# Kernel tuning notes

Measured on AMD Instinct MI355X. Metric: run time of the kernel, lower is better.

Reference implementation:

```python
import jax, jax.numpy as jnp
import numpy as np

N_NODES = 100000
N_EDGES = 1600000
D_IN, D_HID, D_OUT = 128, 128, 40


def _sgconv(feat, W, b, src, dst, n_nodes):
    # DGL SGConv, k=1, norm='both': D^{-1/2} A D^{-1/2} X W + b
    ones = jnp.ones(dst.shape, dtype=feat.dtype)
    deg = jax.ops.segment_sum(ones, dst, num_segments=n_nodes)  # in-degrees
    norm = jnp.clip(deg, 1.0) ** -0.5  # [N]
    h = feat * norm[:, None]
    # sparse aggregation: gather from src, scatter-add to dst
    h = jax.ops.segment_sum(h[src], dst, num_segments=n_nodes)  # [N, d]
    h = h * norm[:, None]
    return h @ W + b


def setup_inputs() -> dict:
    key = jax.random.key(0)
    ks = jax.random.split(key, 6)
    features = jax.random.normal(ks[0], (N_NODES, D_IN), dtype=jnp.float32)
    src = jax.random.randint(ks[1], (N_EDGES,), 0, N_NODES, dtype=jnp.int32)
    dst = jax.random.randint(ks[2], (N_EDGES,), 0, N_NODES, dtype=jnp.int32)
    # Xavier-uniform init like DGL's fc
    lim1 = float(np.sqrt(6.0 / (D_IN + D_HID)))
    lim2 = float(np.sqrt(6.0 / (D_HID + D_OUT)))
    W1 = jax.random.uniform(ks[3], (D_IN, D_HID), jnp.float32, -lim1, lim1)
    b1 = jnp.zeros((D_HID,), dtype=jnp.float32)
    W2 = jax.random.uniform(ks[4], (D_HID, D_OUT), jnp.float32, -lim2, lim2)
    b2 = jnp.zeros((D_OUT,), dtype=jnp.float32)
    return {"features": features, "src": src, "dst": dst,
            "W1": W1, "b1": b1, "W2": W2, "b2": b2, "n_nodes": N_NODES}


def reference(features, src, dst, W1, b1, W2, b2, n_nodes):
    x = _sgconv(features, W1, b1, src, dst, n_nodes)
    x = jax.nn.elu(x)
    x = _sgconv(x, W2, b2, src, dst, n_nodes)
    return x
```

## Files before the change

kernel.cpp:

```cpp
#include <hip/hip_runtime.h>
#include <hip/hip_fp16.h>
#include <math.h>


#define DIN  128
#define DHID 128
#define DOUT 40
#define BSHIFT 9
#define BNODES 512

union U8  { uint2 u; __half2 h[2]; };
union U16 { uint4 u; __half2 h[4]; };

typedef _Float16 f16x8 __attribute__((ext_vector_type(8)));
typedef float    f32x4 __attribute__((ext_vector_type(4)));
union F16X8 { uint4 u; f16x8 f; };
union HCV   { __half h; unsigned short s; };

__device__ __forceinline__ float elu_f(float x) {
    return x > 0.0f ? x : (expf(x) - 1.0f);
}


__global__ void pass1_bucket(const int* __restrict__ src, const int* __restrict__ dst,
                             int E, int NB, int cap,
                             int* __restrict__ bcur, int* __restrict__ bbuf) {
    __shared__ int cnt[256];
    __shared__ int wcur[256];
    const int CHUNK = 8192;
    for (long base = (long)blockIdx.x * CHUNK; base < E; base += (long)gridDim.x * CHUNK) {
        int n = min(CHUNK, (int)(E - base));
        if (threadIdx.x < 256) cnt[threadIdx.x] = 0;
        __syncthreads();
        for (int i = threadIdx.x; i < n; i += blockDim.x) {
            int b = dst[base + i] >> BSHIFT;
            atomicAdd(&cnt[b], 1);
        }
        __syncthreads();
        if (threadIdx.x < NB) {
            int c = cnt[threadIdx.x];
            wcur[threadIdx.x] = (c > 0) ? atomicAdd(&bcur[threadIdx.x], c) : 0;
        }
        __syncthreads();
        for (int i = threadIdx.x; i < n; i += blockDim.x) {
            int s = src[base + i];
            int d = dst[base + i];
            int b = d >> BSHIFT;
            int slot = atomicAdd(&wcur[b], 1);
            if (slot < cap) bbuf[(long)b * cap + slot] = (s << BSHIFT) | (d & (BNODES - 1));
        }
        __syncthreads();
    }
}

__global__ void bucket_scan(const int* __restrict__ bcur, int* __restrict__ bbase, int NB) {
    if (blockIdx.x == 0 && threadIdx.x == 0) {
        int run = 0;
        for (int b = 0; b < NB; ++b) { bbase[b] = run; run += bcur[b]; }
        bbase[NB] = run;
    }
}

__global__ void pass2_sort(const int* __restrict__ bbuf, const int* __restrict__ bcur,
                           const int* __restrict__ bbase, int N, int NB, int cap,
                           float* __restrict__ norm, int* __restrict__ rowptr,
                           int* __restrict__ esrc) {
    __shared__ int cnt[BNODES];
    int b = blockIdx.x;
    int n_b = min(bcur[b], cap);
    int gbase = bbase[b];
    int dbase = b << BSHIFT;
    const int* eb = bbuf + (long)b * cap;
    for (int i = threadIdx.x; i < BNODES; i += blockDim.x) cnt[i] = 0;
    __syncthreads();
    for (int i = threadIdx.x; i < n_b; i += blockDim.x)
        atomicAdd(&cnt[eb[i] & (BNODES - 1)], 1);
    __syncthreads();
    for (int i = threadIdx.x; i < BNODES; i += blockDim.x) {
        int d = dbase + i;
        if (d < N) norm[d] = rsqrtf(fmaxf((float)cnt[i], 1.0f));
    }
    __syncthreads();
    if (threadIdx.x == 0) {
        int run = 0;
        #pragma unroll 4
        for (int i = 0; i < BNODES; ++i) { int c = cnt[i]; cnt[i] = run; run += c; }
    }
    __syncthreads();
    for (int i = threadIdx.x; i < BNODES; i += blockDim.x) {
        int d = dbase + i;
        if (d < N) rowptr[d] = gbase + cnt[i];
    }
    if (b == NB - 1 && threadIdx.x == 0) rowptr[N] = bbase[NB];
    __syncthreads();
    for (int i = threadIdx.x; i < n_b; i += blockDim.x) {
        int v = eb[i];
        int slot = atomicAdd(&cnt[v & (BNODES - 1)], 1);
        esrc[gbase + slot] = ((unsigned)v) >> BSHIFT;
    }
}

__global__ void perm_build(const int* __restrict__ rowptr, int* __restrict__ perm, int N) {
    __shared__ int lcnt[1024];
    __shared__ int lbase[1024];
    const int CHUNK = 4096;
    for (long base = (long)blockIdx.x * CHUNK; base < N; base += (long)gridDim.x * CHUNK) {
        int n = min(CHUNK, (int)(N - base));
        for (int i = threadIdx.x; i < 1024; i += 256) lcnt[i] = 0;
        __syncthreads();
        for (int i = threadIdx.x; i < n; i += 256) {
            int d = min(rowptr[base + i + 1] - rowptr[base + i], 1023);
            atomicAdd(&lcnt[d], 1);
        }
        __syncthreads();
        if (threadIdx.x == 0) {
            int run = 0;
            for (int i = 0; i < 1024; ++i) { int c = lcnt[i]; lbase[i] = run; run += c; }
        }
        __syncthreads();
        for (int i = threadIdx.x; i < 1024; i += 256) lcnt[i] = 0;
        __syncthreads();
        for (int i = threadIdx.x; i < n; i += 256) {
            int d = min(rowptr[base + i + 1] - rowptr[base + i], 1023);
            int pos = lbase[d] + atomicAdd(&lcnt[d], 1);
            perm[base + pos] = base + (int)i;
        }
        __syncthreads();
    }
}

__global__ void norm_from_deg(const int* __restrict__ deg, float* __restrict__ norm, int N) {
    int stride = gridDim.x * blockDim.x;
    for (int i = blockIdx.x * blockDim.x + threadIdx.x; i < N; i += stride)
        norm[i] = rsqrtf(fmaxf((float)deg[i], 1.0f));
}

__global__ void degi_kernel(const int* __restrict__ dst, int E, int* __restrict__ deg) {
    int stride = gridDim.x * blockDim.x;
    for (int i = blockIdx.x * blockDim.x + threadIdx.x; i < E; i += stride)
        atomicAdd(&deg[dst[i]], 1);
}


__global__ void yconv_kernel(const float* __restrict__ feat, const float* __restrict__ norm,
                             __half* __restrict__ y, int N) {
    long total = (long)N * 32;
    long stride = (long)gridDim.x * blockDim.x;
    const float4* f4 = reinterpret_cast<const float4*>(feat);
    uint2* y2 = reinterpret_cast<uint2*>(y);
    for (long i = (long)blockIdx.x * blockDim.x + threadIdx.x; i < total; i += stride) {
        int n = (int)(i >> 5);
        float nm = norm[n];
        float4 v = f4[i];
        U8 o;
        o.h[0] = __floats2half2_rn(v.x * nm, v.y * nm);
        o.h[1] = __floats2half2_rn(v.z * nm, v.w * nm);
        y2[i] = o.u;
    }
}

__global__ void gather1_kernel(const __half* __restrict__ y, const int* __restrict__ rowptr,
                               const int* __restrict__ esrc, const int* __restrict__ perm,
                               const float* __restrict__ norm,
                               __half* __restrict__ aggh, int N) {
    int lane = threadIdx.x & 15;
    long g = ((long)blockIdx.x * blockDim.x + threadIdx.x) >> 4;
    long gstride = ((long)gridDim.x * blockDim.x) >> 4;
    const uint4* y4 = reinterpret_cast<const uint4*>(y);
    uint4* a4 = reinterpret_cast<uint4*>(aggh);
    for (long gi = g; gi < N; gi += gstride) {
        int n = perm[gi];
        int beg = rowptr[n], end = rowptr[n + 1];
        float a0 = 0.f, a1 = 0.f, a2 = 0.f, a3 = 0.f;
        float a4f = 0.f, a5 = 0.f, a6 = 0.f, a7 = 0.f;
        int j = beg;
        for (; j + 1 < end; j += 2) {
            int s0 = esrc[j], s1 = esrc[j + 1];
            U16 u0, u1;
            u0.u = y4[(long)s0 * 16 + lane];
            u1.u = y4[(long)s1 * 16 + lane];
            float2 p0 = __half22float2(u0.h[0]), p1 = __half22float2(u0.h[1]);
            float2 p2 = __half22float2(u0.h[2]), p3 = __half22float2(u0.h[3]);
            float2 q0 = __half22float2(u1.h[0]), q1 = __half22float2(u1.h[1]);
            float2 q2 = __half22float2(u1.h[2]), q3 = __half22float2(u1.h[3]);
            a0 += p0.x + q0.x; a1 += p0.y + q0.y;
            a2 += p1.x + q1.x; a3 += p1.y + q1.y;
            a4f += p2.x + q2.x; a5 += p2.y + q2.y;
            a6 += p3.x + q3.x; a7 += p3.y + q3.y;
        }
        if (j < end) {
            int s0 = esrc[j];
            U16 u0; u0.u = y4[(long)s0 * 16 + lane];
            float2 p0 = __half22float2(u0.h[0]), p1 = __half22float2(u0.h[1]);
            float2 p2 = __half22float2(u0.h[2]), p3 = __half22float2(u0.h[3]);
            a0 += p0.x; a1 += p0.y; a2 += p1.x; a3 += p1.y;
            a4f += p2.x; a5 += p2.y; a6 += p3.x; a7 += p3.y;
        }
        float nm = norm[n];
        U16 o;
        o.h[0] = __floats2half2_rn(a0 * nm, a1 * nm);
        o.h[1] = __floats2half2_rn(a2 * nm, a3 * nm);
        o.h[2] = __floats2half2_rn(a4f * nm, a5 * nm);
        o.h[3] = __floats2half2_rn(a6 * nm, a7 * nm);
        a4[(long)n * 16 + lane] = o.u;
    }
}

__global__ void gather2_kernel(const __half* __restrict__ z, const int* __restrict__ rowptr,
                               const int* __restrict__ esrc, const int* __restrict__ perm,
                               const float* __restrict__ norm, const float* __restrict__ b2,
                               float* __restrict__ out, int N) {
    int lane = threadIdx.x & 7;
    long g = ((long)blockIdx.x * blockDim.x + threadIdx.x) >> 3;
    long gstride = ((long)gridDim.x * blockDim.x) >> 3;
    const uint4* z4 = reinterpret_cast<const uint4*>(z);
    for (long gi = g; gi < N; gi += gstride) {
        int n = perm[gi];
        if (lane < 5) {
            int beg = rowptr[n], end = rowptr[n + 1];
            float a0 = 0.f, a1 = 0.f, a2 = 0.f, a3 = 0.f;
            float a4f = 0.f, a5 = 0.f, a6 = 0.f, a7 = 0.f;
            int j = beg;
            for (; j + 1 < end; j += 2) {
                int s0 = esrc[j], s1 = esrc[j + 1];
                U16 u0, u1;
                u0.u = z4[(long)s0 * 5 + lane];
                u1.u = z4[(long)s1 * 5 + lane];
                float2 p0 = __half22float2(u0.h[0]), p1 = __half22float2(u0.h[1]);
                float2 p2 = __half22float2(u0.h[2]), p3 = __half22float2(u0.h[3]);
                float2 q0 = __half22float2(u1.h[0]), q1 = __half22float2(u1.h[1]);
                float2 q2 = __half22float2(u1.h[2]), q3 = __half22float2(u1.h[3]);
                a0 += p0.x + q0.x; a1 += p0.y + q0.y;
                a2 += p1.x + q1.x; a3 += p1.y + q1.y;
                a4f += p2.x + q2.x; a5 += p2.y + q2.y;
                a6 += p3.x + q3.x; a7 += p3.y + q3.y;
            }
            if (j < end) {
                int s0 = esrc[j];
                U16 u0; u0.u = z4[(long)s0 * 5 + lane];
                float2 p0 = __half22float2(u0.h[0]), p1 = __half22float2(u0.h[1]);
                float2 p2 = __half22float2(u0.h[2]), p3 = __half22float2(u0.h[3]);
                a0 += p0.x; a1 += p0.y; a2 += p1.x; a3 += p1.y;
                a4f += p2.x; a5 += p2.y; a6 += p3.x; a7 += p3.y;
            }
            float nm = norm[n];
            const float4* b4 = reinterpret_cast<const float4*>(b2);
            float4 bb0 = b4[lane * 2], bb1 = b4[lane * 2 + 1];
            float4 o0, o1;
            o0.x = fmaf(a0, nm, bb0.x); o0.y = fmaf(a1, nm, bb0.y);
            o0.z = fmaf(a2, nm, bb0.z); o0.w = fmaf(a3, nm, bb0.w);
            o1.x = fmaf(a4f, nm, bb1.x); o1.y = fmaf(a5, nm, bb1.y);
            o1.z = fmaf(a6, nm, bb1.z); o1.w = fmaf(a7, nm, bb1.w);
            float4* out4 = reinterpret_cast<float4*>(out);
            out4[(long)n * 10 + lane * 2] = o0;
            out4[(long)n * 10 + lane * 2 + 1] = o1;
        }
    }
}


__global__ void wprep_kernel(const float* __restrict__ W1, const float* __restrict__ W2,
                             __half* __restrict__ w1f, __half* __restrict__ w2f) {
    int tid = blockIdx.x * blockDim.x + threadIdx.x;
    if (tid < 2048) {
        int l = tid & 63;
        int t = (tid >> 6) & 3;
        int c = tid >> 8;
        int kb = t * 32 + (l >> 4) * 8, col = c * 16 + (l & 15);
        #pragma unroll
        for (int j = 0; j < 8; ++j)
            w1f[tid * 8 + j] = __float2half_rn(W1[(kb + j) * DHID + col]);
    } else if (tid < 2048 + 768) {
        int id = tid - 2048;
        int l = id & 63;
        int t = (id >> 6) & 3;
        int c = id >> 8;
        int kb = t * 32 + (l >> 4) * 8, col = c * 16 + (l & 15);
        #pragma unroll
        for (int j = 0; j < 8; ++j)
            w2f[id * 8 + j] = (col < DOUT) ? __float2half_rn(W2[(kb + j) * DOUT + col])
                                           : __float2half_rn(0.f);
    }
}

__launch_bounds__(256, 2)
__global__ void mmfused_kernel(const __half* __restrict__ aggh,
                               const __half* __restrict__ w1f, const __half* __restrict__ w2f,
                               const float* __restrict__ b1, const float* __restrict__ norm,
                               __half* __restrict__ z, int N) {
    __shared__ uint4 w1l[2048];
    __shared__ uint4 w2l[768];
    __shared__ unsigned short hl[64 * 128];
    int tid = threadIdx.x;
    const uint4* w1g = reinterpret_cast<const uint4*>(w1f);
    const uint4* w2g = reinterpret_cast<const uint4*>(w2f);
    for (int i = tid; i < 2048; i += 256) w1l[i] = w1g[i];
    for (int i = tid; i < 768; i += 256) w2l[i] = w2g[i];
    __syncthreads();

    int w = tid >> 6, l = tid & 63;
    int lr = l & 15, lg = l >> 4;
    float b1v[8];
    #pragma unroll
    for (int c = 0; c < 8; ++c) b1v[c] = b1[c * 16 + lr];

    int ntiles = (N + 63) >> 6;
    const uint4* ag = reinterpret_cast<const uint4*>(aggh);
    for (int tile = blockIdx.x; tile < ntiles; tile += gridDim.x) {
        int rb = tile << 6;
        int arow = rb + w * 16 + lr;
        int arc = min(arow, N - 1);
        F16X8 af[4];
        #pragma unroll
        for (int t = 0; t < 4; ++t) af[t].u = ag[(long)arc * 16 + t * 4 + lg];
        #pragma unroll
        for (int c = 0; c < 8; ++c) {
            f32x4 acc = {b1v[c], b1v[c], b1v[c], b1v[c]};
            #pragma unroll
            for (int t = 0; t < 4; ++t) {
                F16X8 bf; bf.u = w1l[(c * 4 + t) * 64 + l];
                acc = __builtin_amdgcn_mfma_f32_16x16x32_f16(af[t].f, bf.f, acc, 0, 0, 0);
            }
            int colb2 = (c * 16 + lr) * 2;
            #pragma unroll
            for (int i = 0; i < 4; ++i) {
                int rl = w * 16 + lg * 4 + i;
                HCV cv; cv.h = __float2half_rn(elu_f(acc[i]));
                int ba = (rl * 256 + colb2) ^ ((rl & 7) << 4);
                *reinterpret_cast<unsigned short*>(reinterpret_cast<char*>(hl) + ba) = cv.s;
            }
        }
        int rl2 = w * 16 + lr;
        int sw = (rl2 & 7) << 4;
        F16X8 hf[4];
        #pragma unroll
        for (int t = 0; t < 4; ++t) {
            int ba = (rl2 * 256 + (t * 32 + lg * 8) * 2) ^ sw;
            hf[t].u = *reinterpret_cast<const uint4*>(reinterpret_cast<const char*>(hl) + ba);
        }
        float nmv[4];
        #pragma unroll
        for (int i = 0; i < 4; ++i) {
            int r = rb + w * 16 + lg * 4 + i;
            nmv[i] = norm[min(r, N - 1)];
        }
        #pragma unroll
        for (int c = 0; c < 3; ++c) {
            f32x4 acc = {0.f, 0.f, 0.f, 0.f};
            #pragma unroll
            for (int t = 0; t < 4; ++t) {
                F16X8 bf; bf.u = w2l[(c * 4 + t) * 64 + l];
                acc = __builtin_amdgcn_mfma_f32_16x16x32_f16(hf[t].f, bf.f, acc, 0, 0, 0);
            }
            int col = c * 16 + lr;
            if (col < DOUT) {
                #pragma unroll
                for (int i = 0; i < 4; ++i) {
                    int r = rb + w * 16 + lg * 4 + i;
                    if (r < N) z[(long)r * DOUT + col] = __float2half_rn(acc[i] * nmv[i]);
                }
            }
        }
    }
}


__global__ void scatter1_kernel(const float* __restrict__ feat, const int* __restrict__ src,
                                const int* __restrict__ dst, const float* __restrict__ norm,
                                float* __restrict__ agg, int E) {
    long T = (long)blockIdx.x * blockDim.x + threadIdx.x;
    int l4 = (int)(T & 31);
    long e = T >> 5;
    long estride = ((long)gridDim.x * blockDim.x) >> 5;
    for (; e < E; e += estride) {
        int s = src[e], d = dst[e];
        float ns = norm[s];
        float4 v = reinterpret_cast<const float4*>(feat)[(long)s * 32 + l4];
        float* o = agg + (long)d * DIN + l4 * 4;
        atomicAdd(o + 0, v.x * ns);
        atomicAdd(o + 1, v.y * ns);
        atomicAdd(o + 2, v.z * ns);
        atomicAdd(o + 3, v.w * ns);
    }
}

__global__ void scatter2_kernel(const float* __restrict__ z, const int* __restrict__ src,
                                const int* __restrict__ dst, float* __restrict__ out, int E) {
    long T = (long)blockIdx.x * blockDim.x + threadIdx.x;
    int l = (int)(T & 15);
    long e = T >> 4;
    long estride = ((long)gridDim.x * blockDim.x) >> 4;
    for (; e < E; e += estride) {
        if (l < 10) {
            int s = src[e], d = dst[e];
            float4 v = reinterpret_cast<const float4*>(z)[(long)s * 10 + l];
            float* o = out + (long)d * DOUT + l * 4;
            atomicAdd(o + 0, v.x);
            atomicAdd(o + 1, v.y);
            atomicAdd(o + 2, v.z);
            atomicAdd(o + 3, v.w);
        }
    }
}

__launch_bounds__(256, 2)
__global__ void mm1f_kernel(float* __restrict__ xh, const float* __restrict__ W1,
                            const float* __restrict__ b1, const float* __restrict__ norm,
                            int N) {
    __shared__ float Wl[DIN * DHID];
    __shared__ float Xl[32 * DIN];
    for (int i = threadIdx.x; i < DIN * DHID; i += 256) Wl[i] = W1[i];
    int cg = threadIdx.x & 31;
    int rg = threadIdx.x >> 5;
    int c0 = cg * 4;
    for (long r0 = (long)blockIdx.x * 32; r0 < N; r0 += (long)gridDim.x * 32) {
        __syncthreads();
        for (int i = threadIdx.x; i < 32 * 32; i += 256) {
            int rr = i >> 5;
            long row = r0 + rr;
            float4 v = make_float4(0.f, 0.f, 0.f, 0.f);
            if (row < N) {
                v = reinterpret_cast<const float4*>(xh)[row * 32 + (i & 31)];
                float nm = norm[row];
                v.x *= nm; v.y *= nm; v.z *= nm; v.w *= nm;
            }
            reinterpret_cast<float4*>(Xl)[i] = v;
        }
        __syncthreads();
        float acc[4][4];
        float bx = b1[c0], by = b1[c0 + 1], bz = b1[c0 + 2], bw = b1[c0 + 3];
        #pragma unroll
        for (int r = 0; r < 4; ++r) { acc[r][0] = bx; acc[r][1] = by; acc[r][2] = bz; acc[r][3] = bw; }
        for (int k = 0; k < DIN; k += 4) {
            float4 w0 = *reinterpret_cast<const float4*>(&Wl[(k + 0) * DHID + c0]);
            float4 w1 = *reinterpret_cast<const float4*>(&Wl[(k + 1) * DHID + c0]);
            float4 w2 = *reinterpret_cast<const float4*>(&Wl[(k + 2) * DHID + c0]);
            float4 w3 = *reinterpret_cast<const float4*>(&Wl[(k + 3) * DHID + c0]);
            #pragma unroll
            for (int r = 0; r < 4; ++r) {
                float4 x = *reinterpret_cast<const float4*>(&Xl[(rg * 4 + r) * DIN + k]);
                acc[r][0] = fmaf(x.x, w0.x, fmaf(x.y, w1.x, fmaf(x.z, w2.x, fmaf(x.w, w3.x, acc[r][0]))));
                acc[r][1] = fmaf(x.x, w0.y, fmaf(x.y, w1.y, fmaf(x.z, w2.y, fmaf(x.w, w3.y, acc[r][1]))));
                acc[r][2] = fmaf(x.x, w0.z, fmaf(x.y, w1.z, fmaf(x.z, w2.z, fmaf(x.w, w3.z, acc[r][2]))));
                acc[r][3] = fmaf(x.x, w0.w, fmaf(x.y, w1.w, fmaf(x.z, w2.w, fmaf(x.w, w3.w, acc[r][3]))));
            }
        }
        #pragma unroll
        for (int r = 0; r < 4; ++r) {
            long row = r0 + rg * 4 + r;
            if (row < N) {
                float4 o;
                o.x = elu_f(acc[r][0]); o.y = elu_f(acc[r][1]);
                o.z = elu_f(acc[r][2]); o.w = elu_f(acc[r][3]);
                *reinterpret_cast<float4*>(&xh[row * DIN + c0]) = o;
            }
        }
    }
}

__launch_bounds__(256, 2)
__global__ void mm2f_kernel(const float* __restrict__ h, const float* __restrict__ W2,
                            const float* __restrict__ norm, float* __restrict__ z, int N) {
    __shared__ float Wl[DHID * DOUT];
    __shared__ float Xl[64 * DIN];
    for (int i = threadIdx.x; i < DHID * DOUT; i += 256) Wl[i] = W2[i];
    int cg = threadIdx.x & 15;
    int rg = threadIdx.x >> 4;
    int c0 = cg * 4;
    for (long r0 = (long)blockIdx.x * 64; r0 < N; r0 += (long)gridDim.x * 64) {
        __syncthreads();
        for (int i = threadIdx.x; i < 64 * 32; i += 256) {
            int rr = i >> 5;
            long row = r0 + rr;
            float4 v = make_float4(0.f, 0.f, 0.f, 0.f);
            if (row < N) v = reinterpret_cast<const float4*>(h)[row * 32 + (i & 31)];
            reinterpret_cast<float4*>(Xl)[i] = v;
        }
        __syncthreads();
        if (c0 < DOUT) {
            float acc[4][4];
            #pragma unroll
            for (int r = 0; r < 4; ++r) { acc[r][0] = 0.f; acc[r][1] = 0.f; acc[r][2] = 0.f; acc[r][3] = 0.f; }
            for (int k = 0; k < DHID; k += 4) {
                float4 w0 = *reinterpret_cast<const float4*>(&Wl[(k + 0) * DOUT + c0]);
                float4 w1 = *reinterpret_cast<const float4*>(&Wl[(k + 1) * DOUT + c0]);
                float4 w2 = *reinterpret_cast<const float4*>(&Wl[(k + 2) * DOUT + c0]);
                float4 w3 = *reinterpret_cast<const float4*>(&Wl[(k + 3) * DOUT + c0]);
                #pragma unroll
                for (int r = 0; r < 4; ++r) {
                    float4 x = *reinterpret_cast<const float4*>(&Xl[(rg * 4 + r) * DIN + k]);
                    acc[r][0] = fmaf(x.x, w0.x, fmaf(x.y, w1.x, fmaf(x.z, w2.x, fmaf(x.w, w3.x, acc[r][0]))));
                    acc[r][1] = fmaf(x.x, w0.y, fmaf(x.y, w1.y, fmaf(x.z, w2.y, fmaf(x.w, w3.y, acc[r][1]))));
                    acc[r][2] = fmaf(x.x, w0.z, fmaf(x.y, w1.z, fmaf(x.z, w2.z, fmaf(x.w, w3.z, acc[r][2]))));
                    acc[r][3] = fmaf(x.x, w0.w, fmaf(x.y, w1.w, fmaf(x.z, w2.w, fmaf(x.w, w3.w, acc[r][3]))));
                }
            }
            #pragma unroll
            for (int r = 0; r < 4; ++r) {
                long row = r0 + rg * 4 + r;
                if (row < N) {
                    float nm = norm[row];
                    float4 o;
                    o.x = acc[r][0] * nm; o.y = acc[r][1] * nm;
                    o.z = acc[r][2] * nm; o.w = acc[r][3] * nm;
                    *reinterpret_cast<float4*>(&z[row * DOUT + c0]) = o;
                }
            }
        }
    }
}

__global__ void final_kernel(float* __restrict__ out, const float* __restrict__ norm,
                             const float* __restrict__ b2, int N) {
    long total = (long)N * DOUT;
    long stride = (long)gridDim.x * blockDim.x;
    for (long i = (long)blockIdx.x * blockDim.x + threadIdx.x; i < total; i += stride) {
        int n = (int)(i / DOUT), d = (int)(i % DOUT);
        out[i] = fmaf(out[i], norm[n], b2[d]);
    }
}


static inline size_t al4k(size_t x) { return (x + 4095) & ~(size_t)4095; }

extern "C" void kernel_launch(void* const* d_in, const int* in_sizes, int n_in,
                              void* d_out, int out_size, void* d_ws, size_t ws_size,
                              hipStream_t stream) {
    const float* feat = (const float*)d_in[0];
    const int*   src  = (const int*)d_in[1];
    const int*   dst  = (const int*)d_in[2];
    const float* W1   = (const float*)d_in[3];
    const float* b1   = (const float*)d_in[4];
    const float* W2   = (const float*)d_in[5];
    const float* b2   = (const float*)d_in[6];
    int N = in_sizes[0] / DIN;
    int E = in_sizes[1];
    float* out = (float*)d_out;
    char* ws = (char*)d_ws;

    int NB = (N + BNODES - 1) >> BSHIFT;
    int cap = ((E / (NB > 0 ? NB : 1)) * 5 / 4 + 256 + 1) & ~1;

    size_t o_norm   = 0;
    size_t o_rowptr = o_norm   + al4k((size_t)N * 4);
    size_t o_bcur   = o_rowptr + al4k(((size_t)N + 1) * 4);
    size_t o_bbase  = o_bcur   + al4k((size_t)(NB + 1) * 4);
    size_t o_perm   = o_bbase  + al4k((size_t)(NB + 1) * 4);
    size_t o_esrc   = o_perm   + al4k((size_t)N * 4);
    size_t o_aggh   = o_esrc   + al4k((size_t)E * 4);
    size_t o_y      = o_aggh   + al4k((size_t)N * DIN * 2);
    size_t o_z      = o_y      + al4k((size_t)N * DIN * 2);
    size_t o_w1f    = o_z      + al4k((size_t)N * DOUT * 2);
    size_t o_w2f    = o_w1f    + al4k((size_t)16384 * 2);
    size_t need     = o_w2f    + al4k((size_t)6144 * 2);

    bool bb_fits = (size_t)NB * cap * 4 <= (size_t)N * DIN * 2;
    bool packs   = N <= (1 << 22);

    if (ws_size >= need && NB <= 256 && bb_fits && packs) {
        float*  norm   = (float*)(ws + o_norm);
        int*    rowptr = (int*)(ws + o_rowptr);
        int*    bcur   = (int*)(ws + o_bcur);
        int*    bbase  = (int*)(ws + o_bbase);
        int*    perm   = (int*)(ws + o_perm);
        int*    esrc   = (int*)(ws + o_esrc);
        __half* aggh   = (__half*)(ws + o_aggh);
        int*    bbuf   = (int*)(ws + o_aggh);
        __half* y      = (__half*)(ws + o_y);
        __half* z      = (__half*)(ws + o_z);
        __half* w1f    = (__half*)(ws + o_w1f);
        __half* w2f    = (__half*)(ws + o_w2f);

        hipMemsetAsync(bcur, 0, (size_t)(NB + 1) * 4, stream);

        wprep_kernel<<<11, 256, 0, stream>>>(W1, W2, w1f, w2f);
        int p1grid = (E + 8191) / 8192;
        pass1_bucket<<<p1grid, 256, 0, stream>>>(src, dst, E, NB, cap, bcur, bbuf);
        bucket_scan<<<1, 1, 0, stream>>>(bcur, bbase, NB);
        pass2_sort<<<NB, 256, 0, stream>>>(bbuf, bcur, bbase, N, NB, cap, norm, rowptr, esrc);
        perm_build<<<(N + 4095) / 4096, 256, 0, stream>>>(rowptr, perm, N);
        yconv_kernel<<<4096, 256, 0, stream>>>(feat, norm, y, N);

        gather1_kernel<<<(N * 16 + 255) / 256, 256, 0, stream>>>(y, rowptr, esrc, perm, norm, aggh, N);
        mmfused_kernel<<<512, 256, 0, stream>>>(aggh, w1f, w2f, b1, norm, z, N);
        gather2_kernel<<<(N * 8 + 255) / 256, 256, 0, stream>>>(z, rowptr, esrc, perm, norm, b2, out, N);
    } else {
        size_t f_norm = 0;
        size_t f_agg  = f_norm + al4k((size_t)N * 4);
        size_t f_z    = f_agg  + al4k((size_t)N * DIN * 4);
        float* norm = (float*)(ws + f_norm);
        float* agg  = (float*)(ws + f_agg);
        float* z    = (float*)(ws + f_z);
        int*   degi = (int*)(ws + f_norm);

        hipMemsetAsync(degi, 0, (size_t)N * 4, stream);
        hipMemsetAsync(agg, 0, (size_t)N * DIN * 4, stream);
        hipMemsetAsync(d_out, 0, (size_t)N * DOUT * 4, stream);

        degi_kernel<<<1024, 256, 0, stream>>>(dst, E, degi);
        norm_from_deg<<<(N + 255) / 256, 256, 0, stream>>>(degi, (float*)degi, N);
        scatter1_kernel<<<4096, 256, 0, stream>>>(feat, src, dst, norm, agg, E);
        mm1f_kernel<<<(N + 31) / 32, 256, 0, stream>>>(agg, W1, b1, norm, N);
        mm2f_kernel<<<(N + 63) / 64, 256, 0, stream>>>(agg, W2, norm, z, N);
        scatter2_kernel<<<4096, 256, 0, stream>>>(z, src, dst, out, E);
        final_kernel<<<4096, 256, 0, stream>>>(out, norm, b2, N);
    }
}
```

Before: 238.7 us.

## Fuse degree-sorted perm into pass2, repack gather2 lanes, add nontemporal stores

Builds the per-bucket degree-sorted node permutation inside pass2_sort with a second shared histogram, which removes the separate perm_build kernel and its extra pass over rowptr. gather2 now packs 12 five-lane node groups into each 64-lane wavefront instead of using 8-lane groups where three lanes sit idle, so fewer wavefronts are launched. Output stores from the gathers become nontemporal. Sorting now happens within 512-node buckets rather than 4096-node chunks, and degrees are capped at 255, so load balancing across wavefronts may be coarser.

```diff
diff --git a/kernel.cpp b/kernel.cpp
--- a/kernel.cpp
+++ b/kernel.cpp
@@ -12,10 +12,13 @@
 union U8  { uint2 u; __half2 h[2]; };
 union U16 { uint4 u; __half2 h[4]; };
 
-typedef _Float16 f16x8 __attribute__((ext_vector_type(8)));
-typedef float    f32x4 __attribute__((ext_vector_type(4)));
+typedef _Float16     f16x8 __attribute__((ext_vector_type(8)));
+typedef float        f32x4 __attribute__((ext_vector_type(4)));
+typedef unsigned int u32x4 __attribute__((ext_vector_type(4)));
 union F16X8 { uint4 u; f16x8 f; };
 union HCV   { __half h; unsigned short s; };
+union UV4   { uint4 h; u32x4 v; };
+union FV4   { float4 h; f32x4 v; };
 
 __device__ __forceinline__ float elu_f(float x) {
     return x > 0.0f ? x : (expf(x) - 1.0f);
@@ -64,68 +67,46 @@
 __global__ void pass2_sort(const int* __restrict__ bbuf, const int* __restrict__ bcur,
                            const int* __restrict__ bbase, int N, int NB, int cap,
                            float* __restrict__ norm, int* __restrict__ rowptr,
-                           int* __restrict__ esrc) {
+                           int* __restrict__ esrc, int* __restrict__ perm) {
     __shared__ int cnt[BNODES];
+    __shared__ int dcnt[256];
+    int tid = threadIdx.x;
     int b = blockIdx.x;
     int n_b = min(bcur[b], cap);
     int gbase = bbase[b];
     int dbase = b << BSHIFT;
     const int* eb = bbuf + (long)b * cap;
-    for (int i = threadIdx.x; i < BNODES; i += blockDim.x) cnt[i] = 0;
+    cnt[tid] = 0; cnt[tid + 256] = 0; dcnt[tid] = 0;
     __syncthreads();
-    for (int i = threadIdx.x; i < n_b; i += blockDim.x)
+    for (int i = tid; i < n_b; i += 256)
         atomicAdd(&cnt[eb[i] & (BNODES - 1)], 1);
     __syncthreads();
-    for (int i = threadIdx.x; i < BNODES; i += blockDim.x) {
-        int d = dbase + i;
-        if (d < N) norm[d] = rsqrtf(fmaxf((float)cnt[i], 1.0f));
-    }
+    int d0 = cnt[tid], d1 = cnt[tid + 256];
+    bool v0 = (dbase + tid) < N, v1 = (dbase + tid + 256) < N;
+    if (v0) norm[dbase + tid] = rsqrtf(fmaxf((float)d0, 1.0f));
+    if (v1) norm[dbase + tid + 256] = rsqrtf(fmaxf((float)d1, 1.0f));
+    if (v0) atomicAdd(&dcnt[min(d0, 255)], 1);
+    if (v1) atomicAdd(&dcnt[min(d1, 255)], 1);
     __syncthreads();
-    if (threadIdx.x == 0) {
+    if (tid == 0) {
         int run = 0;
         #pragma unroll 4
         for (int i = 0; i < BNODES; ++i) { int c = cnt[i]; cnt[i] = run; run += c; }
+        run = 0;
+        #pragma unroll 4
+        for (int i = 0; i < 256; ++i) { int c = dcnt[i]; dcnt[i] = run; run += c; }
     }
     __syncthreads();
-    for (int i = threadIdx.x; i < BNODES; i += blockDim.x) {
-        int d = dbase + i;
-        if (d < N) rowptr[d] = gbase + cnt[i];
-    }
-    if (b == NB - 1 && threadIdx.x == 0) rowptr[N] = bbase[NB];
+    if (v0) rowptr[dbase + tid] = gbase + cnt[tid];
+    if (v1) rowptr[dbase + tid + 256] = gbase + cnt[tid + 256];
+    if (b == NB - 1 && tid == 0) rowptr[N] = bbase[NB];
+    if (v0) { int p = atomicAdd(&dcnt[min(d0, 255)], 1); perm[dbase + p] = dbase + tid; }
+    if (v1) { int p = atomicAdd(&dcnt[min(d1, 255)], 1); perm[dbase + p] = dbase + tid + 256; }
     __syncthreads();
-    for (int i = threadIdx.x; i < n_b; i += blockDim.x) {
+    for (int i = tid; i < n_b; i += 256) {
         int v = eb[i];
         int slot = atomicAdd(&cnt[v & (BNODES - 1)], 1);
         esrc[gbase + slot] = ((unsigned)v) >> BSHIFT;
-    }
-}
-
-__global__ void perm_build(const int* __restrict__ rowptr, int* __restrict__ perm, int N) {
-    __shared__ int lcnt[1024];
-    __shared__ int lbase[1024];
-    const int CHUNK = 4096;
-    for (long base = (long)blockIdx.x * CHUNK; base < N; base += (long)gridDim.x * CHUNK) {
-        int n = min(CHUNK, (int)(N - base));
-        for (int i = threadIdx.x; i < 1024; i += 256) lcnt[i] = 0;
-        __syncthreads();
-        for (int i = threadIdx.x; i < n; i += 256) {
-            int d = min(rowptr[base + i + 1] - rowptr[base + i], 1023);
-            atomicAdd(&lcnt[d], 1);
-        }
-        __syncthreads();
-        if (threadIdx.x == 0) {
-            int run = 0;
-            for (int i = 0; i < 1024; ++i) { int c = lcnt[i]; lbase[i] = run; run += c; }
-        }
-        __syncthreads();
-        for (int i = threadIdx.x; i < 1024; i += 256) lcnt[i] = 0;
-        __syncthreads();
-        for (int i = threadIdx.x; i < n; i += 256) {
-            int d = min(rowptr[base + i + 1] - rowptr[base + i], 1023);
-            int pos = lbase[d] + atomicAdd(&lcnt[d], 1);
-            perm[base + pos] = base + (int)i;
-        }
-        __syncthreads();
     }
 }
 
@@ -167,7 +148,7 @@
     long g = ((long)blockIdx.x * blockDim.x + threadIdx.x) >> 4;
     long gstride = ((long)gridDim.x * blockDim.x) >> 4;
     const uint4* y4 = reinterpret_cast<const uint4*>(y);
-    uint4* a4 = reinterpret_cast<uint4*>(aggh);
+    u32x4* a4 = reinterpret_cast<u32x4*>(aggh);
     for (long gi = g; gi < N; gi += gstride) {
         int n = perm[gi];
         int beg = rowptr[n], end = rowptr[n + 1];
@@ -202,7 +183,8 @@
         o.h[1] = __floats2half2_rn(a2 * nm, a3 * nm);
         o.h[2] = __floats2half2_rn(a4f * nm, a5 * nm);
         o.h[3] = __floats2half2_rn(a6 * nm, a7 * nm);
-        a4[(long)n * 16 + lane] = o.u;
+        UV4 ov; ov.h = o.u;
+        __builtin_nontemporal_store(ov.v, &a4[(long)n * 16 + lane]);
     }
 }
 
@@ -210,13 +192,17 @@
                                const int* __restrict__ esrc, const int* __restrict__ perm,
                                const float* __restrict__ norm, const float* __restrict__ b2,
                                float* __restrict__ out, int N) {
-    int lane = threadIdx.x & 7;
-    long g = ((long)blockIdx.x * blockDim.x + threadIdx.x) >> 3;
-    long gstride = ((long)gridDim.x * blockDim.x) >> 3;
+    int lane = threadIdx.x & 63;
+    int grp = lane / 5;
+    int seg = lane - grp * 5;
+    bool act = grp < 12;
+    long wglob = ((long)blockIdx.x * blockDim.x + threadIdx.x) >> 6;
+    long g0 = wglob * 12 + grp;
+    long gstride = (((long)gridDim.x * blockDim.x) >> 6) * 12;
     const uint4* z4 = reinterpret_cast<const uint4*>(z);
-    for (long gi = g; gi < N; gi += gstride) {
-        int n = perm[gi];
-        if (lane < 5) {
+    for (long gi = g0; gi < N; gi += gstride) {
+        if (act) {
+            int n = perm[gi];
             int beg = rowptr[n], end = rowptr[n + 1];
             float a0 = 0.f, a1 = 0.f, a2 = 0.f, a3 = 0.f;
             float a4f = 0.f, a5 = 0.f, a6 = 0.f, a7 = 0.f;
@@ -224,8 +210,8 @@
             for (; j + 1 < end; j += 2) {
                 int s0 = esrc[j], s1 = esrc[j + 1];
                 U16 u0, u1;
-                u0.u = z4[(long)s0 * 5 + lane];
-                u1.u = z4[(long)s1 * 5 + lane];
+                u0.u = z4[(long)s0 * 5 + seg];
+                u1.u = z4[(long)s1 * 5 + seg];
                 float2 p0 = __half22float2(u0.h[0]), p1 = __half22float2(u0.h[1]);
                 float2 p2 = __half22float2(u0.h[2]), p3 = __half22float2(u0.h[3]);
                 float2 q0 = __half22float2(u1.h[0]), q1 = __half22float2(u1.h[1]);
@@ -237,7 +223,7 @@
             }
             if (j < end) {
                 int s0 = esrc[j];
-                U16 u0; u0.u = z4[(long)s0 * 5 + lane];
+                U16 u0; u0.u = z4[(long)s0 * 5 + seg];
                 float2 p0 = __half22float2(u0.h[0]), p1 = __half22float2(u0.h[1]);
                 float2 p2 = __half22float2(u0.h[2]), p3 = __half22float2(u0.h[3]);
                 a0 += p0.x; a1 += p0.y; a2 += p1.x; a3 += p1.y;
@@ -245,15 +231,15 @@
             }
             float nm = norm[n];
             const float4* b4 = reinterpret_cast<const float4*>(b2);
-            float4 bb0 = b4[lane * 2], bb1 = b4[lane * 2 + 1];
-            float4 o0, o1;
-            o0.x = fmaf(a0, nm, bb0.x); o0.y = fmaf(a1, nm, bb0.y);
-            o0.z = fmaf(a2, nm, bb0.z); o0.w = fmaf(a3, nm, bb0.w);
-            o1.x = fmaf(a4f, nm, bb1.x); o1.y = fmaf(a5, nm, bb1.y);
-            o1.z = fmaf(a6, nm, bb1.z); o1.w = fmaf(a7, nm, bb1.w);
-            float4* out4 = reinterpret_cast<float4*>(out);
-            out4[(long)n * 10 + lane * 2] = o0;
-            out4[(long)n * 10 + lane * 2 + 1] = o1;
+            float4 bb0 = b4[seg * 2], bb1 = b4[seg * 2 + 1];
+            FV4 o0, o1;
+            o0.h.x = fmaf(a0, nm, bb0.x); o0.h.y = fmaf(a1, nm, bb0.y);
+            o0.h.z = fmaf(a2, nm, bb0.z); o0.h.w = fmaf(a3, nm, bb0.w);
+            o1.h.x = fmaf(a4f, nm, bb1.x); o1.h.y = fmaf(a5, nm, bb1.y);
+            o1.h.z = fmaf(a6, nm, bb1.z); o1.h.w = fmaf(a7, nm, bb1.w);
+            f32x4* out4 = reinterpret_cast<f32x4*>(out);
+            __builtin_nontemporal_store(o0.v, &out4[(long)n * 10 + seg * 2]);
+            __builtin_nontemporal_store(o1.v, &out4[(long)n * 10 + seg * 2 + 1]);
         }
     }
 }
@@ -577,13 +563,12 @@
         int p1grid = (E + 8191) / 8192;
         pass1_bucket<<<p1grid, 256, 0, stream>>>(src, dst, E, NB, cap, bcur, bbuf);
         bucket_scan<<<1, 1, 0, stream>>>(bcur, bbase, NB);
-        pass2_sort<<<NB, 256, 0, stream>>>(bbuf, bcur, bbase, N, NB, cap, norm, rowptr, esrc);
-        perm_build<<<(N + 4095) / 4096, 256, 0, stream>>>(rowptr, perm, N);
+        pass2_sort<<<NB, 256, 0, stream>>>(bbuf, bcur, bbase, N, NB, cap, norm, rowptr, esrc, perm);
         yconv_kernel<<<4096, 256, 0, stream>>>(feat, norm, y, N);
 
         gather1_kernel<<<(N * 16 + 255) / 256, 256, 0, stream>>>(y, rowptr, esrc, perm, norm, aggh, N);
         mmfused_kernel<<<512, 256, 0, stream>>>(aggh, w1f, w2f, b1, norm, z, N);
-        gather2_kernel<<<(N * 8 + 255) / 256, 256, 0, stream>>>(z, rowptr, esrc, perm, norm, b2, out, N);
+        gather2_kernel<<<(N + 47) / 48, 256, 0, stream>>>(z, rowptr, esrc, perm, norm, b2, out, N);
     } else {
         size_t f_norm = 0;
         size_t f_agg  = f_norm + al4k((size_t)N * 4);
```

New measurement: 241.3 us. Within noise of the previous version (+1.1%).
